# Optimization experiments

Hardware: AMD Instinct MI355X
Metric: run time of the kernel (lower is better)

The kernel has to match this reference:

```python
import jax, jax.numpy as jnp
import numpy as np

B, S, E, H, V, OOV = 128, 400, 512, 512, 50257, 50
VEXT = V + OOV


def setup_inputs() -> dict:
    key = jax.random.key(0)
    ks = jax.random.split(key, 20)
    w = lambda k, shp: (0.02 * jax.random.normal(k, shp)).astype(jnp.float32)
    return {
        'input_emb': jax.random.normal(ks[0], (B, 1, E), jnp.float32),
        'input_feed': jax.random.normal(ks[1], (B, 1, H), jnp.float32),
        'hidden': jax.random.normal(ks[2], (1, B, H), jnp.float32),
        'context': jax.random.normal(ks[3], (1, B, H), jnp.float32),
        'states': jax.random.normal(ks[4], (B, S, H), jnp.float32),
        'states_features': jax.random.normal(ks[5], (B, S, H), jnp.float32),
        'source_mask': jnp.ones((B, S), jnp.float32),
        'coverage': jnp.zeros((B, S), jnp.float32),
        'source_ids': jax.random.randint(ks[6], (B, S), 0, VEXT, jnp.int32),
        'W_ic': w(ks[7], (E, H + E)), 'b_ic': jnp.zeros((E,), jnp.float32),
        'W_ih': w(ks[8], (4 * H, E)), 'W_hh': w(ks[9], (4 * H, H)),
        'b_ih': jnp.zeros((4 * H,), jnp.float32), 'b_hh': jnp.zeros((4 * H,), jnp.float32),
        'W_dec': w(ks[10], (H, H)), 'b_att': jnp.zeros((H,), jnp.float32),
        'v_att': w(ks[11], (H,)), 'w_c': w(ks[12], (1,)),
        'W_out': w(ks[13], (H, 2 * H)), 'b_out': jnp.zeros((H,), jnp.float32),
        'W_pg': w(ks[14], (1, H)), 'b_pg': jnp.zeros((1,), jnp.float32),
        'W_v': w(ks[15], (V, H)), 'b_v': jnp.zeros((V,), jnp.float32),
    }


def reference(input_emb, input_feed, hidden, context, states, states_features,
              source_mask, coverage, source_ids,
              W_ic, b_ic, W_ih, W_hh, b_ih, b_hh,
              W_dec, b_att, v_att, w_c, W_out, b_out,
              W_pg, b_pg, W_v, b_v):
    # x = input_context(cat(input_emb, input_feed))  -> [B,1,E]
    x = jnp.concatenate([input_emb, input_feed], axis=2) @ W_ic.T + b_ic
    # single LSTM step (PyTorch gate order i,f,g,o)
    h0, c0 = hidden[0], context[0]                      # [B,H]
    gates = x[:, 0] @ W_ih.T + b_ih + h0 @ W_hh.T + b_hh
    i, f, g, o = jnp.split(gates, 4, axis=-1)
    i, f, o = jax.nn.sigmoid(i), jax.nn.sigmoid(f), jax.nn.sigmoid(o)
    c1 = f * c0 + i * jnp.tanh(g)
    h1 = o * jnp.tanh(c1)                               # rnn_output [B,H]
    # coverage attention
    dec_fea = h1 @ W_dec.T + b_att                      # [B,H]
    e = jnp.tanh(states_features + dec_fea[:, None, :] + w_c * coverage[..., None]) @ v_att  # [B,S]
    e = jnp.where(source_mask > 0, e, jnp.float32(-1e9))
    attn = jax.nn.softmax(e, axis=-1) * source_mask
    attn = attn / (attn.sum(-1, keepdims=True) + 1e-12)  # [B,S]
    ctx = jnp.einsum('bs,bsh->bh', attn, states)
    dec_out = jnp.concatenate([h1, ctx], axis=-1) @ W_out.T + b_out  # decoder_output [B,H]
    coverage_new = coverage + attn
    # pointer-generator mixing
    p_gen = jax.nn.sigmoid(dec_out @ W_pg.T + b_pg)     # [B,1]
    vocab_dist = p_gen * jax.nn.softmax(dec_out @ W_v.T + b_v, axis=-1)  # [B,V]
    ext = jnp.zeros((B, VEXT), vocab_dist.dtype).at[:, :V].set(vocab_dist)
    attn_dist = (1.0 - p_gen) * attn                    # [B,S]
    final = ext.at[jnp.arange(B)[:, None], source_ids].add(attn_dist)  # scatter_add over vocab
    final_dist = final[:, None, :]                      # [B,1,VEXT]
    return (final_dist, p_gen, attn, coverage_new, h1[None], c1[None], dec_out[:, None, :])
```

## Files before the change

kernel.cpp:

```cpp
#include <hip/hip_runtime.h>
#include <hip/hip_bf16.h>

#define B_   128
#define S_   400
#define H_   512
#define V_   50257
#define VX_  50307

#define OFF_FINAL 0
#define OFF_PGEN  6439296
#define OFF_ATTN  6439424
#define OFF_COV   6490624
#define OFF_H1    6541824
#define OFF_C1    6607360
#define OFF_DEC   6672896

typedef __attribute__((ext_vector_type(8))) short bf16x8;
typedef __attribute__((ext_vector_type(4))) float f32x4;

static __device__ __forceinline__ float sigmoid_f(float x) {
    return 1.0f / (1.0f + __expf(-x));
}
static __device__ __forceinline__ float tanh_f(float x) {
    return 1.0f - 2.0f / (__expf(2.0f * x) + 1.0f);
}
static __device__ __forceinline__ unsigned int pk2(float x, float y) {
    union { __hip_bfloat162 h; unsigned int u; } cv;
    cv.h = __float22bfloat162_rn(make_float2(x, y));
    return cv.u;
}

__global__ __launch_bounds__(256) void zero_ws(
    float4* __restrict__ ws4, float4* __restrict__ dec4)
{
    const int i = blockIdx.x * 256 + threadIdx.x;
    const float4 z = make_float4(0.f, 0.f, 0.f, 0.f);
    if (i < 98336) ws4[i] = z;
    if (i < 16384) dec4[i] = z;
}

template <int NT>
__global__ __launch_bounds__(256) void gemm_mfma(
    const float* __restrict__ A1, const float* __restrict__ W1, int ldw1, int kwo1,
    const float* __restrict__ A2, const float* __restrict__ W2, int ldw2, int kwo2,
    const float* __restrict__ bias1,
    float* __restrict__ C, int N,
    const float* __restrict__ wpg, float* __restrict__ pgen_acc)
{
    __shared__ __align__(16) unsigned short As[128 * 40];
    __shared__ __align__(16) unsigned short Ws[NT * 16 * 40];
    const int tid  = threadIdx.x;
    const int bn0  = blockIdx.x * (NT * 16);
    const int lane = tid & 63;
    const int wv   = tid >> 6;
    const int quad = lane >> 4;
    const int col  = lane & 15;

    f32x4 acc[2][NT];
#pragma unroll
    for (int i = 0; i < 2; ++i)
#pragma unroll
        for (int j = 0; j < NT; ++j) acc[i][j] = (f32x4){0.f, 0.f, 0.f, 0.f};

    const int ar = tid >> 1;
    const int ac = (tid & 1) << 4;
    const int wr = (NT == 8) ? (tid >> 1) : (tid >> 2);
    const int wc = (NT == 8) ? ((tid & 1) << 4) : ((tid & 3) << 3);
    const int wrg = (bn0 + wr < N) ? (bn0 + wr) : (N - 1);

    const int Ktot = (A2 != nullptr) ? 1024 : 512;
    const int KC   = Ktot / gridDim.y;
    const int kg0  = blockIdx.y * KC;
    const int nsteps = KC >> 5;

    const float* ApB[2];
    const float* WpB[2];
    ApB[0] = A1 + (long)ar * 512 + ac;
    WpB[0] = W1 + (long)wrg * ldw1 + kwo1 + wc;
    ApB[1] = A2 ? (A2 + (long)ar * 512 + ac) : ApB[0];
    WpB[1] = W2 ? (W2 + (long)wrg * ldw2 + kwo2 + wc) : WpB[0];

    float4 aC[4], wC[NT / 2], aN[4], wN[NT / 2];

    auto fetch = [&](int s, float4* a, float4* w) {
        const int kg = kg0 + (s << 5);
        const int ph = kg >> 9;
        const int k0 = kg & 511;
        const float* Ap = ApB[ph] + k0;
        const float* Wp = WpB[ph] + k0;
#pragma unroll
        for (int i = 0; i < 4; ++i) a[i] = *(const float4*)(Ap + i * 4);
#pragma unroll
        for (int i = 0; i < NT / 2; ++i) w[i] = *(const float4*)(Wp + i * 4);
    };

    fetch(0, aC, wC);
    for (int s = 0; s < nsteps; ++s) {
        __syncthreads();
        uint4* apd = (uint4*)&As[ar * 40 + ac];
        apd[0] = make_uint4(pk2(aC[0].x, aC[0].y), pk2(aC[0].z, aC[0].w),
                            pk2(aC[1].x, aC[1].y), pk2(aC[1].z, aC[1].w));
        apd[1] = make_uint4(pk2(aC[2].x, aC[2].y), pk2(aC[2].z, aC[2].w),
                            pk2(aC[3].x, aC[3].y), pk2(aC[3].z, aC[3].w));
        uint4* wpd = (uint4*)&Ws[wr * 40 + wc];
        wpd[0] = make_uint4(pk2(wC[0].x, wC[0].y), pk2(wC[0].z, wC[0].w),
                            pk2(wC[1].x, wC[1].y), pk2(wC[1].z, wC[1].w));
        if (NT == 8)
            wpd[1] = make_uint4(pk2(wC[2].x, wC[2].y), pk2(wC[2].z, wC[2].w),
                                pk2(wC[3].x, wC[3].y), pk2(wC[3].z, wC[3].w));
        __syncthreads();

        if (s + 1 < nsteps) fetch(s + 1, aN, wN);

        const bf16x8 aF0 = *(const bf16x8*)&As[(wv * 32 + col) * 40 + quad * 8];
        const bf16x8 aF1 = *(const bf16x8*)&As[(wv * 32 + 16 + col) * 40 + quad * 8];
#pragma unroll
        for (int ni = 0; ni < NT; ++ni) {
            const bf16x8 bF = *(const bf16x8*)&Ws[(ni * 16 + col) * 40 + quad * 8];
            acc[0][ni] = __builtin_amdgcn_mfma_f32_16x16x32_bf16(aF0, bF, acc[0][ni], 0, 0, 0);
            acc[1][ni] = __builtin_amdgcn_mfma_f32_16x16x32_bf16(aF1, bF, acc[1][ni], 0, 0, 0);
        }
#pragma unroll
        for (int i = 0; i < 4; ++i) aC[i] = aN[i];
#pragma unroll
        for (int i = 0; i < NT / 2; ++i) wC[i] = wN[i];
    }

    const bool split = (gridDim.y > 1);
    const bool addb  = (!split) || (blockIdx.y == 0);

    float pgp[2][4];
#pragma unroll
    for (int i = 0; i < 2; ++i)
#pragma unroll
        for (int r = 0; r < 4; ++r) pgp[i][r] = 0.f;

#pragma unroll
    for (int mi = 0; mi < 2; ++mi) {
#pragma unroll
        for (int ni = 0; ni < NT; ++ni) {
            const int n = bn0 + ni * 16 + col;
            if (n < N) {
                const float bv = addb ? bias1[n] : 0.f;
                const float wpv = wpg ? wpg[n] : 0.f;
#pragma unroll
                for (int r = 0; r < 4; ++r) {
                    const int m = wv * 32 + mi * 16 + quad * 4 + r;
                    const float v = acc[mi][ni][r] + bv;
                    if (split) atomicAdd(&C[(long)m * N + n], v);
                    else       C[(long)m * N + n] = v;
                    pgp[mi][r] += v * wpv;
                }
            }
        }
    }
    if (wpg) {
#pragma unroll
        for (int mi = 0; mi < 2; ++mi)
#pragma unroll
            for (int r = 0; r < 4; ++r) {
                float v = pgp[mi][r];
                v += __shfl_xor(v, 1); v += __shfl_xor(v, 2);
                v += __shfl_xor(v, 4); v += __shfl_xor(v, 8);
                if (col == 0) {
                    const int m = wv * 32 + mi * 16 + quad * 4 + r;
                    atomicAdd(&pgen_acc[m], v);
                }
            }
    }
}

__global__ __launch_bounds__(256) void pack_a(
    const float* __restrict__ A, unsigned short* __restrict__ Apk)
{
    const int u  = blockIdx.x * 256 + threadIdx.x;
    const int c  = u & 15;
    const int q  = (u >> 4) & 3;
    const int mt = (u >> 6) & 7;
    const int sl = u >> 9;
    const float* src = A + (long)(mt * 16 + c) * 512 + sl * 32 + q * 8;
    const float4 x = *(const float4*)src;
    const float4 y = *(const float4*)(src + 4);
    *(uint4*)(Apk + (long)u * 8) = make_uint4(pk2(x.x, x.y), pk2(x.z, x.w),
                                              pk2(y.x, y.y), pk2(y.z, y.w));
}

__global__ __launch_bounds__(256, 2) void vocab_gemm(
    const unsigned short* __restrict__ Apk, const float* __restrict__ W,
    const float* __restrict__ bias, float* __restrict__ C, int N,
    float* __restrict__ pm, float* __restrict__ ps, int nbn)
{
    __shared__ __align__(16) unsigned short Ws[64 * 512];
    const int tid  = threadIdx.x;
    const int lane = tid & 63;
    const int w    = tid >> 6;
    const int quad = lane >> 4;
    const int c    = lane & 15;
    const int nb   = blockIdx.x;

#pragma unroll
    for (int i = 0; i < 16; ++i) {
        const int r  = i * 4 + w;
        const int rg = (nb * 64 + r < N) ? (nb * 64 + r) : (N - 1);
        const int k  = lane << 3;
        const float* src = W + (long)rg * 512 + k;
        const float4 x = *(const float4*)src;
        const float4 y = *(const float4*)(src + 4);
        const int a16 = (r << 6) + (lane ^ (r & 7));
        *(uint4*)&Ws[a16 << 3] = make_uint4(pk2(x.x, x.y), pk2(x.z, x.w),
                                            pk2(y.x, y.y), pk2(y.z, y.w));
    }

    f32x4 acc[8];
#pragma unroll
    for (int mt = 0; mt < 8; ++mt) acc[mt] = (f32x4){0.f, 0.f, 0.f, 0.f};

    bf16x8 aA[8], aB[8];
    auto loadA = [&](int sl, bf16x8* dst) {
#pragma unroll
        for (int mt = 0; mt < 8; ++mt) {
            const long u = (((long)(sl * 8 + mt) * 4 + quad) << 4) + c;
            dst[mt] = *(const bf16x8*)(Apk + u * 8);
        }
    };
    loadA(0, aA);
    __syncthreads();

#pragma unroll
    for (int sl = 0; sl < 16; ++sl) {
        bf16x8* cur = (sl & 1) ? aB : aA;
        bf16x8* nxt = (sl & 1) ? aA : aB;
        if (sl + 1 < 16) loadA(sl + 1, nxt);
        const int a16 = ((w * 16 + c) << 6) + (((sl << 2) + quad) ^ (c & 7));
        const bf16x8 bF = *(const bf16x8*)&Ws[a16 << 3];
#pragma unroll
        for (int mt = 0; mt < 8; ++mt)
            acc[mt] = __builtin_amdgcn_mfma_f32_16x16x32_bf16(cur[mt], bF, acc[mt], 0, 0, 0);
    }

    __syncthreads();
    float* redM = (float*)Ws;
    float* redS = (float*)Ws + 512;
    const int n  = nb * 64 + w * 16 + c;
    const bool ok = (n < N);
    const float bv = bias[ok ? n : (N - 1)];
#pragma unroll
    for (int mt = 0; mt < 8; ++mt) {
#pragma unroll
        for (int r = 0; r < 4; ++r) {
            const float v = acc[mt][r] + bv;
            const int m = mt * 16 + quad * 4 + r;
            if (ok) C[(long)m * N + n] = v;
            float mx = ok ? v : -3.0e38f;
            mx = fmaxf(mx, __shfl_xor(mx, 1));
            mx = fmaxf(mx, __shfl_xor(mx, 2));
            mx = fmaxf(mx, __shfl_xor(mx, 4));
            mx = fmaxf(mx, __shfl_xor(mx, 8));
            float sv = ok ? __expf(v - mx) : 0.f;
            sv += __shfl_xor(sv, 1); sv += __shfl_xor(sv, 2);
            sv += __shfl_xor(sv, 4); sv += __shfl_xor(sv, 8);
            if (c == 0) {
                redM[m * 4 + w] = mx;
                redS[m * 4 + w] = sv;
            }
        }
    }
    __syncthreads();
    if (tid < 128) {
        float M = -3.0e38f;
#pragma unroll
        for (int j = 0; j < 4; ++j) M = fmaxf(M, redM[tid * 4 + j]);
        float S = 0.f;
#pragma unroll
        for (int j = 0; j < 4; ++j) S += redS[tid * 4 + j] * __expf(redM[tid * 4 + j] - M);
        pm[(long)tid * nbn + nb] = M;
        ps[(long)tid * nbn + nb] = S;
    }
}

__global__ __launch_bounds__(256) void lstm_cell(
    const float* __restrict__ gates, const float* __restrict__ bhh,
    const float* __restrict__ c0,
    float* __restrict__ h1, float* __restrict__ c1)
{
    const int idx = blockIdx.x * 256 + threadIdx.x;
    const int m = idx >> 9;
    const int h = idx & 511;
    const float* g = gates + (long)m * 2048;
    const float iv = sigmoid_f(g[h]        + bhh[h]);
    const float fv = sigmoid_f(g[512 + h]  + bhh[512 + h]);
    const float gv = tanh_f   (g[1024 + h] + bhh[1024 + h]);
    const float ov = sigmoid_f(g[1536 + h] + bhh[1536 + h]);
    const float c = fv * c0[idx] + iv * gv;
    c1[idx] = c;
    h1[idx] = ov * tanh_f(c);
}

__global__ __launch_bounds__(256) void attn_scores(
    const float* __restrict__ sfeat, const float* __restrict__ decfea,
    const float* __restrict__ cov, const float* __restrict__ wc,
    const float* __restrict__ vatt, float* __restrict__ e)
{
    const int lane = threadIdx.x & 63;
    const int pair = blockIdx.x * 4 + (threadIdx.x >> 6);
    const int b = pair / 400;
    const float cc = wc[0] * cov[pair];
    const float* sp = sfeat + ((long)pair << 9) + (lane << 3);
    const float* dp = decfea + (b << 9) + (lane << 3);
    const float* vp = vatt + (lane << 3);
    const float4 s0 = *(const float4*)sp, s1 = *(const float4*)(sp + 4);
    const float4 d0 = *(const float4*)dp, d1 = *(const float4*)(dp + 4);
    const float4 v0 = *(const float4*)vp, v1 = *(const float4*)(vp + 4);
    float acc = tanh_f(s0.x + d0.x + cc) * v0.x
              + tanh_f(s0.y + d0.y + cc) * v0.y
              + tanh_f(s0.z + d0.z + cc) * v0.z
              + tanh_f(s0.w + d0.w + cc) * v0.w
              + tanh_f(s1.x + d1.x + cc) * v1.x
              + tanh_f(s1.y + d1.y + cc) * v1.y
              + tanh_f(s1.z + d1.z + cc) * v1.z
              + tanh_f(s1.w + d1.w + cc) * v1.w;
#pragma unroll
    for (int off = 32; off > 0; off >>= 1) acc += __shfl_down(acc, off);
    if (lane == 0) e[pair] = acc;
}

__global__ __launch_bounds__(256) void attn_softmax(
    const float* __restrict__ e, const float* __restrict__ mask,
    const float* __restrict__ cov,
    float* __restrict__ attn, float* __restrict__ covnew, float* __restrict__ ctx)
{
    __shared__ float sm[4], sps[4], spms[4];
    const int b = blockIdx.x, tid = threadIdx.x;
    ctx[(b << 9) + tid] = 0.f;
    ctx[(b << 9) + 256 + tid] = 0.f;

    float vals[2], msk[2];
    float m = -3.0e38f;
#pragma unroll
    for (int it = 0; it < 2; ++it) {
        const int s = tid + (it << 8);
        float mk = 0.f, v = -3.0e38f;
        if (s < 400) {
            mk = mask[b * 400 + s];
            v = (mk > 0.f) ? e[b * 400 + s] : -1.0e9f;
        }
        vals[it] = v; msk[it] = mk;
        m = fmaxf(m, v);
    }
#pragma unroll
    for (int off = 32; off > 0; off >>= 1) m = fmaxf(m, __shfl_down(m, off));
    if ((tid & 63) == 0) sm[tid >> 6] = m;
    __syncthreads();
    const float M = fmaxf(fmaxf(sm[0], sm[1]), fmaxf(sm[2], sm[3]));

    float p[2], sp = 0.f, spm = 0.f;
#pragma unroll
    for (int it = 0; it < 2; ++it) {
        const int s = tid + (it << 8);
        float pv = 0.f;
        if (s < 400) pv = __expf(vals[it] - M);
        p[it] = pv; sp += pv; spm += pv * msk[it];
    }
#pragma unroll
    for (int off = 32; off > 0; off >>= 1) {
        sp += __shfl_down(sp, off);
        spm += __shfl_down(spm, off);
    }
    if ((tid & 63) == 0) { sps[tid >> 6] = sp; spms[tid >> 6] = spm; }
    __syncthreads();
    const float SP = sps[0] + sps[1] + sps[2] + sps[3];
    const float SPM = spms[0] + spms[1] + spms[2] + spms[3];
    const float inv = 1.0f / (SPM + 1e-12f * SP);
#pragma unroll
    for (int it = 0; it < 2; ++it) {
        const int s = tid + (it << 8);
        if (s < 400) {
            const float a = p[it] * msk[it] * inv;
            attn[b * 400 + s] = a;
            covnew[b * 400 + s] = cov[b * 400 + s] + a;
        }
    }
}

__global__ __launch_bounds__(256) void ctx_kernel(
    const float* __restrict__ attn, const float* __restrict__ states,
    float* __restrict__ ctx)
{
    const int bx = blockIdx.x;
    const int b = bx >> 2, chunk = bx & 3;
    const int tid = threadIdx.x;
    const int c = tid & 127;
    const int sh = tid >> 7;
    const int s0 = chunk * 100 + sh;
    const float* base = states + (long)b * 400 * 512;
    float4 acc = make_float4(0.f, 0.f, 0.f, 0.f);
    for (int i = 0; i < 50; ++i) {
        const int s = s0 + (i << 1);
        const float a = attn[b * 400 + s];
        const float4 st = *(const float4*)(base + (long)s * 512 + (c << 2));
        acc.x = fmaf(a, st.x, acc.x);
        acc.y = fmaf(a, st.y, acc.y);
        acc.z = fmaf(a, st.z, acc.z);
        acc.w = fmaf(a, st.w, acc.w);
    }
    float* cp = ctx + (b << 9) + (c << 2);
    atomicAdd(cp + 0, acc.x);
    atomicAdd(cp + 1, acc.y);
    atomicAdd(cp + 2, acc.z);
    atomicAdd(cp + 3, acc.w);
}

__global__ __launch_bounds__(256) void final_write(
    const float* __restrict__ logits, const float* __restrict__ pm,
    const float* __restrict__ ps, const float* __restrict__ pgen_acc,
    const float* __restrict__ bpg, float* __restrict__ final,
    float* __restrict__ o_pgen, int nblk)
{
    __shared__ float sred[4];
    __shared__ float sM, sS;
    const int b = blockIdx.y;
    const int tid = threadIdx.x;
    const float* pmb = pm + (long)b * nblk;
    const float* psb = ps + (long)b * nblk;

    float m = -3.0e38f;
    for (int i = tid; i < nblk; i += 256) m = fmaxf(m, pmb[i]);
#pragma unroll
    for (int off = 32; off > 0; off >>= 1) m = fmaxf(m, __shfl_down(m, off));
    if ((tid & 63) == 0) sred[tid >> 6] = m;
    __syncthreads();
    if (tid == 0) sM = fmaxf(fmaxf(sred[0], sred[1]), fmaxf(sred[2], sred[3]));
    __syncthreads();
    const float M = sM;

    float s = 0.f;
    for (int i = tid; i < nblk; i += 256) s += psb[i] * __expf(pmb[i] - M);
#pragma unroll
    for (int off = 32; off > 0; off >>= 1) s += __shfl_down(s, off);
    if ((tid & 63) == 0) sred[tid >> 6] = s;
    __syncthreads();
    if (tid == 0) sS = sred[0] + sred[1] + sred[2] + sred[3];
    __syncthreads();
    const float S = sS;

    const float pg = sigmoid_f(pgen_acc[b] + bpg[0]);
    if (blockIdx.x == 0 && tid == 0) o_pgen[b] = pg;

    const int v0 = (blockIdx.x * 256 + tid) << 2;
    if (v0 >= VX_) return;
    const float sc = pg / S;
    const float* row = logits + (long)b * V_;
    float* out = final + (long)b * VX_ + v0;
#pragma unroll
    for (int j = 0; j < 4; ++j) {
        const int v = v0 + j;
        if (v < VX_) out[j] = (v < V_) ? __expf(row[v] - M) * sc : 0.f;
    }
}

__global__ __launch_bounds__(256) void scatter_kernel(
    const int* __restrict__ ids, const float* __restrict__ attn,
    const float* __restrict__ pgen, float* __restrict__ final)
{
    const int s = blockIdx.x * 256 + threadIdx.x;
    const int b = blockIdx.y;
    if (s < 400) {
        const float v = (1.0f - pgen[b]) * attn[b * 400 + s];
        atomicAdd(final + (long)b * VX_ + ids[b * 400 + s], v);
    }
}

extern "C" void kernel_launch(void* const* d_in, const int* in_sizes, int n_in,
                              void* d_out, int out_size, void* d_ws, size_t ws_size,
                              hipStream_t stream)
{
    const float* input_emb  = (const float*)d_in[0];
    const float* input_feed = (const float*)d_in[1];
    const float* hidden     = (const float*)d_in[2];
    const float* context    = (const float*)d_in[3];
    const float* states     = (const float*)d_in[4];
    const float* sfeat      = (const float*)d_in[5];
    const float* mask       = (const float*)d_in[6];
    const float* cov        = (const float*)d_in[7];
    const int*   src_ids    = (const int*)d_in[8];
    const float* W_ic  = (const float*)d_in[9];
    const float* b_ic  = (const float*)d_in[10];
    const float* W_ih  = (const float*)d_in[11];
    const float* W_hh  = (const float*)d_in[12];
    const float* b_ih  = (const float*)d_in[13];
    const float* b_hh  = (const float*)d_in[14];
    const float* W_dec = (const float*)d_in[15];
    const float* b_att = (const float*)d_in[16];
    const float* v_att = (const float*)d_in[17];
    const float* w_c   = (const float*)d_in[18];
    const float* W_out = (const float*)d_in[19];
    const float* b_out = (const float*)d_in[20];
    const float* W_pg  = (const float*)d_in[21];
    const float* b_pg  = (const float*)d_in[22];
    const float* W_v   = (const float*)d_in[23];
    const float* b_v   = (const float*)d_in[24];

    float* out = (float*)d_out;
    float* o_final = out + OFF_FINAL;
    float* o_pgen  = out + OFF_PGEN;
    float* o_attn  = out + OFF_ATTN;
    float* o_cov   = out + OFF_COV;
    float* o_h1    = out + OFF_H1;
    float* o_c1    = out + OFF_C1;
    float* o_dec   = out + OFF_DEC;

    float* ws = (float*)d_ws;
    float* w_x      = ws;
    float* w_decfea = ws + 65536;
    float* w_gates  = ws + 131072;
    float* w_pga    = ws + 393216;
    float* w_e      = ws + 393344;
    float* w_ctx    = ws + 444544;
    float* w_logits = ws + 510080;
    float* w_pm     = ws + 6942976;
    float* w_ps     = ws + 7043584;
    unsigned short* w_apk = (unsigned short*)w_gates;

    const dim3 blk(256);
    zero_ws<<<385, blk, 0, stream>>>((float4*)ws, (float4*)o_dec);
    gemm_mfma<4><<<dim3(8, 8), blk, 0, stream>>>(
        input_emb, W_ic, 1024, 0, input_feed, W_ic, 1024, 512,
        b_ic, w_x, 512, nullptr, nullptr);
    gemm_mfma<4><<<dim3(32, 4), blk, 0, stream>>>(
        w_x, W_ih, 512, 0, hidden, W_hh, 512, 0,
        b_ih, w_gates, 2048, nullptr, nullptr);
    lstm_cell<<<256, blk, 0, stream>>>(w_gates, b_hh, context, o_h1, o_c1);
    gemm_mfma<4><<<dim3(8, 4), blk, 0, stream>>>(
        o_h1, W_dec, 512, 0, nullptr, nullptr, 0, 0,
        b_att, w_decfea, 512, nullptr, nullptr);
    attn_scores<<<12800, blk, 0, stream>>>(sfeat, w_decfea, cov, w_c, v_att, w_e);
    attn_softmax<<<128, blk, 0, stream>>>(w_e, mask, cov, o_attn, o_cov, w_ctx);
    ctx_kernel<<<512, blk, 0, stream>>>(o_attn, states, w_ctx);
    gemm_mfma<4><<<dim3(8, 8), blk, 0, stream>>>(
        o_h1, W_out, 1024, 0, w_ctx, W_out, 1024, 512,
        b_out, o_dec, 512, W_pg, w_pga);
    pack_a<<<32, blk, 0, stream>>>(o_dec, w_apk);
    vocab_gemm<<<786, blk, 0, stream>>>(
        w_apk, W_v, b_v, w_logits, V_, w_pm, w_ps, 786);
    final_write<<<dim3(50, 128), blk, 0, stream>>>(w_logits, w_pm, w_ps, w_pga,
                                                   b_pg, o_final, o_pgen, 786);
    scatter_kernel<<<dim3(2, 128), blk, 0, stream>>>(src_ids, o_attn, o_pgen, o_final);
}
```

Before: 472.6 us.

## Shrink vocab GEMM tile to 32 columns, split warps over M, add row-merge kernel

The vocab GEMM now gives each block 32 vocabulary columns instead of 64, doubling the grid to 1571 blocks. Each warp handles 32 batch rows by 32 columns instead of all 128 rows by 16 columns, and the LDS buffer halves so more blocks can stay resident per CU. The per-block partial max and sum are written straight from registers without a cross-warp LDS reduction. A new row_merge kernel reduces the partials once per row, so each of the 6400 final_write blocks no longer redoes that reduction. The cost is twice as many partial entries, one extra launch, and a rearranged workspace.

```diff
diff --git a/kernel.cpp b/kernel.cpp
--- a/kernel.cpp
+++ b/kernel.cpp
@@ -6,6 +6,7 @@
 #define H_   512
 #define V_   50257
 #define VX_  50307
+#define NBN_ 1571
 
 #define OFF_FINAL 0
 #define OFF_PGEN  6439296
@@ -31,12 +32,13 @@
 }
 
 __global__ __launch_bounds__(256) void zero_ws(
-    float4* __restrict__ ws4, float4* __restrict__ dec4)
+    float4* __restrict__ ws4, float4* __restrict__ dec4, float4* __restrict__ pga4)
 {
     const int i = blockIdx.x * 256 + threadIdx.x;
     const float4 z = make_float4(0.f, 0.f, 0.f, 0.f);
-    if (i < 98336) ws4[i] = z;
+    if (i < 98304) ws4[i] = z;
     if (i < 16384) dec4[i] = z;
+    if (i < 32)    pga4[i] = z;
 }
 
 template <int NT>
@@ -185,12 +187,12 @@
                                               pk2(y.x, y.y), pk2(y.z, y.w));
 }
 
-__global__ __launch_bounds__(256, 2) void vocab_gemm(
+__global__ __launch_bounds__(256, 5) void vocab_gemm(
     const unsigned short* __restrict__ Apk, const float* __restrict__ W,
     const float* __restrict__ bias, float* __restrict__ C, int N,
     float* __restrict__ pm, float* __restrict__ ps, int nbn)
 {
-    __shared__ __align__(16) unsigned short Ws[64 * 512];
+    __shared__ __align__(16) unsigned short Ws[32 * 512];
     const int tid  = threadIdx.x;
     const int lane = tid & 63;
     const int w    = tid >> 6;
@@ -199,11 +201,10 @@
     const int nb   = blockIdx.x;
 
 #pragma unroll
-    for (int i = 0; i < 16; ++i) {
+    for (int i = 0; i < 8; ++i) {
         const int r  = i * 4 + w;
-        const int rg = (nb * 64 + r < N) ? (nb * 64 + r) : (N - 1);
-        const int k  = lane << 3;
-        const float* src = W + (long)rg * 512 + k;
+        const int rg = (nb * 32 + r < N) ? (nb * 32 + r) : (N - 1);
+        const float* src = W + (long)rg * 512 + (lane << 3);
         const float4 x = *(const float4*)src;
         const float4 y = *(const float4*)(src + 4);
         const int a16 = (r << 6) + (lane ^ (r & 7));
@@ -211,16 +212,18 @@
                                             pk2(y.x, y.y), pk2(y.z, y.w));
     }
 
-    f32x4 acc[8];
-#pragma unroll
-    for (int mt = 0; mt < 8; ++mt) acc[mt] = (f32x4){0.f, 0.f, 0.f, 0.f};
-
-    bf16x8 aA[8], aB[8];
+    f32x4 acc[2][2];
+#pragma unroll
+    for (int mi = 0; mi < 2; ++mi)
+#pragma unroll
+        for (int nj = 0; nj < 2; ++nj) acc[mi][nj] = (f32x4){0.f, 0.f, 0.f, 0.f};
+
+    bf16x8 aA[2], aB[2];
     auto loadA = [&](int sl, bf16x8* dst) {
 #pragma unroll
-        for (int mt = 0; mt < 8; ++mt) {
-            const long u = (((long)(sl * 8 + mt) * 4 + quad) << 4) + c;
-            dst[mt] = *(const bf16x8*)(Apk + u * 8);
+        for (int mi = 0; mi < 2; ++mi) {
+            const int u = ((sl * 8 + (w * 2 + mi)) * 4 + quad) * 16 + c;
+            dst[mi] = *(const bf16x8*)(Apk + (long)u * 8);
         }
     };
     loadA(0, aA);
@@ -231,50 +234,74 @@
         bf16x8* cur = (sl & 1) ? aB : aA;
         bf16x8* nxt = (sl & 1) ? aA : aB;
         if (sl + 1 < 16) loadA(sl + 1, nxt);
-        const int a16 = ((w * 16 + c) << 6) + (((sl << 2) + quad) ^ (c & 7));
-        const bf16x8 bF = *(const bf16x8*)&Ws[a16 << 3];
-#pragma unroll
-        for (int mt = 0; mt < 8; ++mt)
-            acc[mt] = __builtin_amdgcn_mfma_f32_16x16x32_bf16(cur[mt], bF, acc[mt], 0, 0, 0);
-    }
-
-    __syncthreads();
-    float* redM = (float*)Ws;
-    float* redS = (float*)Ws + 512;
-    const int n  = nb * 64 + w * 16 + c;
-    const bool ok = (n < N);
-    const float bv = bias[ok ? n : (N - 1)];
-#pragma unroll
-    for (int mt = 0; mt < 8; ++mt) {
+        const int uk = ((sl << 2) + quad) ^ (c & 7);
+        const bf16x8 bF0 = *(const bf16x8*)&Ws[((c << 6) + uk) << 3];
+        const bf16x8 bF1 = *(const bf16x8*)&Ws[((((16 + c)) << 6) + uk) << 3];
+        acc[0][0] = __builtin_amdgcn_mfma_f32_16x16x32_bf16(cur[0], bF0, acc[0][0], 0, 0, 0);
+        acc[0][1] = __builtin_amdgcn_mfma_f32_16x16x32_bf16(cur[0], bF1, acc[0][1], 0, 0, 0);
+        acc[1][0] = __builtin_amdgcn_mfma_f32_16x16x32_bf16(cur[1], bF0, acc[1][0], 0, 0, 0);
+        acc[1][1] = __builtin_amdgcn_mfma_f32_16x16x32_bf16(cur[1], bF1, acc[1][1], 0, 0, 0);
+    }
+
+    const int n0 = nb * 32 + c;
+    const int n1 = nb * 32 + 16 + c;
+    const bool ok0 = (n0 < N), ok1 = (n1 < N);
+    const float bv0 = bias[ok0 ? n0 : (N - 1)];
+    const float bv1 = bias[ok1 ? n1 : (N - 1)];
+#pragma unroll
+    for (int mi = 0; mi < 2; ++mi) {
 #pragma unroll
         for (int r = 0; r < 4; ++r) {
-            const float v = acc[mt][r] + bv;
-            const int m = mt * 16 + quad * 4 + r;
-            if (ok) C[(long)m * N + n] = v;
-            float mx = ok ? v : -3.0e38f;
+            const int m = w * 32 + mi * 16 + quad * 4 + r;
+            const float v0 = acc[mi][0][r] + bv0;
+            const float v1 = acc[mi][1][r] + bv1;
+            if (ok0) C[(long)m * N + n0] = v0;
+            if (ok1) C[(long)m * N + n1] = v1;
+            float mx = fmaxf(ok0 ? v0 : -3.0e38f, ok1 ? v1 : -3.0e38f);
             mx = fmaxf(mx, __shfl_xor(mx, 1));
             mx = fmaxf(mx, __shfl_xor(mx, 2));
             mx = fmaxf(mx, __shfl_xor(mx, 4));
             mx = fmaxf(mx, __shfl_xor(mx, 8));
-            float sv = ok ? __expf(v - mx) : 0.f;
+            float sv = (ok0 ? __expf(v0 - mx) : 0.f) + (ok1 ? __expf(v1 - mx) : 0.f);
             sv += __shfl_xor(sv, 1); sv += __shfl_xor(sv, 2);
             sv += __shfl_xor(sv, 4); sv += __shfl_xor(sv, 8);
             if (c == 0) {
-                redM[m * 4 + w] = mx;
-                redS[m * 4 + w] = sv;
+                pm[(long)m * nbn + nb] = mx;
+                ps[(long)m * nbn + nb] = sv;
             }
         }
     }
+}
+
+__global__ __launch_bounds__(256) void row_merge(
+    const float* __restrict__ pm, const float* __restrict__ ps, int nblk,
+    float* __restrict__ Mrow, float* __restrict__ Srow)
+{
+    __shared__ float sred[4];
+    __shared__ float sM;
+    const int b = blockIdx.x, tid = threadIdx.x;
+    const float* pmb = pm + (long)b * nblk;
+    const float* psb = ps + (long)b * nblk;
+
+    float m = -3.0e38f;
+    for (int i = tid; i < nblk; i += 256) m = fmaxf(m, pmb[i]);
+#pragma unroll
+    for (int off = 32; off > 0; off >>= 1) m = fmaxf(m, __shfl_down(m, off));
+    if ((tid & 63) == 0) sred[tid >> 6] = m;
     __syncthreads();
-    if (tid < 128) {
-        float M = -3.0e38f;
-#pragma unroll
-        for (int j = 0; j < 4; ++j) M = fmaxf(M, redM[tid * 4 + j]);
-        float S = 0.f;
-#pragma unroll
-        for (int j = 0; j < 4; ++j) S += redS[tid * 4 + j] * __expf(redM[tid * 4 + j] - M);
-        pm[(long)tid * nbn + nb] = M;
-        ps[(long)tid * nbn + nb] = S;
+    if (tid == 0) sM = fmaxf(fmaxf(sred[0], sred[1]), fmaxf(sred[2], sred[3]));
+    __syncthreads();
+    const float M = sM;
+
+    float s = 0.f;
+    for (int i = tid; i < nblk; i += 256) s += psb[i] * __expf(pmb[i] - M);
+#pragma unroll
+    for (int off = 32; off > 0; off >>= 1) s += __shfl_down(s, off);
+    if ((tid & 63) == 0) sred[tid >> 6] = s;
+    __syncthreads();
+    if (tid == 0) {
+        Mrow[b] = M;
+        Srow[b] = sred[0] + sred[1] + sred[2] + sred[3];
     }
 }
 
@@ -411,38 +438,15 @@
 }
 
 __global__ __launch_bounds__(256) void final_write(
-    const float* __restrict__ logits, const float* __restrict__ pm,
-    const float* __restrict__ ps, const float* __restrict__ pgen_acc,
+    const float* __restrict__ logits, const float* __restrict__ Mrow,
+    const float* __restrict__ Srow, const float* __restrict__ pgen_acc,
     const float* __restrict__ bpg, float* __restrict__ final,
-    float* __restrict__ o_pgen, int nblk)
-{
-    __shared__ float sred[4];
-    __shared__ float sM, sS;
+    float* __restrict__ o_pgen)
+{
     const int b = blockIdx.y;
     const int tid = threadIdx.x;
-    const float* pmb = pm + (long)b * nblk;
-    const float* psb = ps + (long)b * nblk;
-
-    float m = -3.0e38f;
-    for (int i = tid; i < nblk; i += 256) m = fmaxf(m, pmb[i]);
-#pragma unroll
-    for (int off = 32; off > 0; off >>= 1) m = fmaxf(m, __shfl_down(m, off));
-    if ((tid & 63) == 0) sred[tid >> 6] = m;
-    __syncthreads();
-    if (tid == 0) sM = fmaxf(fmaxf(sred[0], sred[1]), fmaxf(sred[2], sred[3]));
-    __syncthreads();
-    const float M = sM;
-
-    float s = 0.f;
-    for (int i = tid; i < nblk; i += 256) s += psb[i] * __expf(pmb[i] - M);
-#pragma unroll
-    for (int off = 32; off > 0; off >>= 1) s += __shfl_down(s, off);
-    if ((tid & 63) == 0) sred[tid >> 6] = s;
-    __syncthreads();
-    if (tid == 0) sS = sred[0] + sred[1] + sred[2] + sred[3];
-    __syncthreads();
-    const float S = sS;
-
+    const float M = Mrow[b];
+    const float S = Srow[b];
     const float pg = sigmoid_f(pgen_acc[b] + bpg[0]);
     if (blockIdx.x == 0 && tid == 0) o_pgen[b] = pg;
 
@@ -513,16 +517,18 @@
     float* w_x      = ws;
     float* w_decfea = ws + 65536;
     float* w_gates  = ws + 131072;
-    float* w_pga    = ws + 393216;
+    float* w_pm     = ws;
+    float* w_ps     = ws + 201088;
     float* w_e      = ws + 393344;
     float* w_ctx    = ws + 444544;
     float* w_logits = ws + 510080;
-    float* w_pm     = ws + 6942976;
-    float* w_ps     = ws + 7043584;
-    unsigned short* w_apk = (unsigned short*)w_gates;
+    unsigned short* w_apk = (unsigned short*)(ws + 6942976);
+    float* w_Mrow   = ws + 6975744;
+    float* w_Srow   = ws + 6975872;
+    float* w_pga    = ws + 6976000;
 
     const dim3 blk(256);
-    zero_ws<<<385, blk, 0, stream>>>((float4*)ws, (float4*)o_dec);
+    zero_ws<<<385, blk, 0, stream>>>((float4*)ws, (float4*)o_dec, (float4*)w_pga);
     gemm_mfma<4><<<dim3(8, 8), blk, 0, stream>>>(
         input_emb, W_ic, 1024, 0, input_feed, W_ic, 1024, 512,
         b_ic, w_x, 512, nullptr, nullptr);
@@ -540,9 +546,10 @@
         o_h1, W_out, 1024, 0, w_ctx, W_out, 1024, 512,
         b_out, o_dec, 512, W_pg, w_pga);
     pack_a<<<32, blk, 0, stream>>>(o_dec, w_apk);
-    vocab_gemm<<<786, blk, 0, stream>>>(
-        w_apk, W_v, b_v, w_logits, V_, w_pm, w_ps, 786);
-    final_write<<<dim3(50, 128), blk, 0, stream>>>(w_logits, w_pm, w_ps, w_pga,
-                                                   b_pg, o_final, o_pgen, 786);
+    vocab_gemm<<<NBN_, blk, 0, stream>>>(
+        w_apk, W_v, b_v, w_logits, V_, w_pm, w_ps, NBN_);
+    row_merge<<<128, blk, 0, stream>>>(w_pm, w_ps, NBN_, w_Mrow, w_Srow);
+    final_write<<<dim3(50, 128), blk, 0, stream>>>(w_logits, w_Mrow, w_Srow,
+                                                   w_pga, b_pg, o_final, o_pgen);
     scatter_kernel<<<dim3(2, 128), blk, 0, stream>>>(src_ids, o_attn, o_pgen, o_final);
 }
```

Result: faster. 446.7 us (-5.5%).
